# Optimization experiments

Measured on AMD Instinct MI355X. Metric: run time of the kernel, lower is better.

## Reference

```python
import jax, jax.numpy as jnp
import numpy as np

HIDDEN = 1024
HEADS = 16
HEAD_DIM = HIDDEN // HEADS


def setup_inputs() -> dict:
    key = jax.random.key(0)
    ks = jax.random.split(key, 5)
    B, T = 4, 2048
    x = jax.random.normal(ks[0], (B, T, HIDDEN), dtype=jnp.float32)
    s = 1.0 / np.sqrt(HIDDEN)
    qkv_w = jax.random.normal(ks[1], (HIDDEN, 3 * HIDDEN), dtype=jnp.float32) * s
    qkv_b = jnp.zeros((3 * HIDDEN,), dtype=jnp.float32)
    proj_w = jax.random.normal(ks[2], (HIDDEN, HIDDEN), dtype=jnp.float32) * s
    proj_b = jnp.zeros((HIDDEN,), dtype=jnp.float32)
    return {"x": x, "qkv_w": qkv_w, "qkv_b": qkv_b, "proj_w": proj_w, "proj_b": proj_b}


def reference(x, qkv_w, qkv_b, proj_w, proj_b):
    B, T, C = x.shape
    qkv = x @ qkv_w + qkv_b                       # [B,T,3C]
    qkv = qkv.reshape(B, T, 3, HEADS, HEAD_DIM)
    q, k, v = qkv[:, :, 0], qkv[:, :, 1], qkv[:, :, 2]  # [B,T,H,D]
    scale = HEAD_DIM ** -0.5
    scores = jnp.einsum('bthd,bshd->bhts', q, k) * scale  # [B,H,T,T]
    attn = jax.nn.softmax(scores, axis=-1)
    out = jnp.einsum('bhts,bshd->bthd', attn, v).reshape(B, T, C)
    return out @ proj_w + proj_b
```

## Files before the change

### kernel.cpp

```cpp
#include <hip/hip_runtime.h>
#include <hip/hip_bf16.h>

#define HID  1024
#define N3   3072
#define NH   16
#define HD   64
#define SEQ  2048
#define NB   4
#define MTOT 8192

typedef unsigned short u16x8 __attribute__((ext_vector_type(8)));
typedef unsigned short u16x4 __attribute__((ext_vector_type(4)));
typedef float f32x4 __attribute__((ext_vector_type(4)));

static __device__ __forceinline__ unsigned short f2bf(float f) {
    union { float f; unsigned u; } v; v.f = f;
    unsigned r = (v.u + 0x7fffu + ((v.u >> 16) & 1u)) >> 16;
    return (unsigned short)r;
}

static __device__ __forceinline__ float fexp2(float x) {
    float r; asm("v_exp_f32 %0, %1" : "=v"(r) : "v"(x)); return r;
}

typedef __attribute__((address_space(3))) void* lds_vp;
typedef const __attribute__((address_space(1))) void* gbl_vp;

static __device__ __forceinline__ void gload16(const void* g, void* l) {
    __builtin_amdgcn_global_load_lds((gbl_vp)g, (lds_vp)l, 16, 0, 0);
}

#define CQ 0.18033688011112042f

__global__ void k_cvt(const float* __restrict__ in, unsigned short* __restrict__ out, int n) {
    int i = (blockIdx.x * 256 + threadIdx.x) * 8;
    if (i >= n) return;
    float4 a = *(const float4*)(in + i);
    float4 b = *(const float4*)(in + i + 4);
    u16x8 p;
    p[0]=f2bf(a.x); p[1]=f2bf(a.y); p[2]=f2bf(a.z); p[3]=f2bf(a.w);
    p[4]=f2bf(b.x); p[5]=f2bf(b.y); p[6]=f2bf(b.z); p[7]=f2bf(b.w);
    *(u16x8*)(out + i) = p;
}

__global__ void k_tcvt(const float* __restrict__ W, unsigned short* __restrict__ WT, int R, int C) {
    int tiles_c = C >> 6;
    int k0 = (blockIdx.x / tiles_c) << 6;
    int n0 = (blockIdx.x % tiles_c) << 6;
    __shared__ unsigned short tile[64 * 64];
    int tid = threadIdx.x;
    #pragma unroll
    for (int it = 0; it < 2; ++it) {
        int task = it * 256 + tid;
        int t = task >> 3, dc = task & 7;
        const float* src = W + (size_t)(k0 + t) * C + n0 + dc * 8;
        float4 a = *(const float4*)src;
        float4 b = *(const float4*)(src + 4);
        u16x8 p;
        p[0]=f2bf(a.x); p[1]=f2bf(a.y); p[2]=f2bf(a.z); p[3]=f2bf(a.w);
        p[4]=f2bf(b.x); p[5]=f2bf(b.y); p[6]=f2bf(b.z); p[7]=f2bf(b.w);
        *(u16x8*)&tile[t * 64 + ((dc ^ (t & 7)) << 3)] = p;
    }
    __syncthreads();
    #pragma unroll
    for (int it = 0; it < 2; ++it) {
        int task = it * 256 + tid;
        int d = task >> 3, tc = task & 7;
        u16x8 p;
        #pragma unroll
        for (int i = 0; i < 8; ++i) {
            int ii = (i + tc) & 7;
            int t = tc * 8 + ii;
            p[ii] = tile[t * 64 + ((((d >> 3) ^ (t & 7)) << 3)) + (d & 7)];
        }
        *(u16x8*)(WT + (size_t)(n0 + d) * R + k0 + tc * 8) = p;
    }
}

template<int MODE>
__global__ __launch_bounds__(256) void k_gemm(const unsigned short* __restrict__ A,
                                              const unsigned short* __restrict__ BT,
                                              const float* __restrict__ bias,
                                              void* __restrict__ C1, void* __restrict__ C2,
                                              int M, int N, int K) {
    int tiles_n = N >> 7;
    int bid = (blockIdx.x & 7) * (gridDim.x >> 3) + (blockIdx.x >> 3);
    int bm = bid / tiles_n, bn = bid % tiles_n;
    int tid = threadIdx.x, wid = tid >> 6, lane = tid & 63;
    int wr = wid >> 1, wc = wid & 1;
    int fr = lane & 15, fg = lane >> 4;

    __shared__ unsigned short lA[128 * 64];
    __shared__ unsigned short lB[128 * 64];

    f32x4 acc[4][4];
    #pragma unroll
    for (int m = 0; m < 4; ++m)
        #pragma unroll
        for (int n = 0; n < 4; ++n)
            acc[m][n] = (f32x4){0.f, 0.f, 0.f, 0.f};

    int srow = lane >> 3;
    int sch  = (lane & 7) ^ srow;
    const unsigned short* aSrc[4]; const unsigned short* bSrc[4];
    unsigned short* aDst[4]; unsigned short* bDst[4];
    #pragma unroll
    for (int i = 0; i < 4; ++i) {
        int rbase = i * 32 + wid * 8;
        aSrc[i] = A  + (size_t)(bm * 128 + rbase + srow) * K + sch * 8;
        bSrc[i] = BT + (size_t)(bn * 128 + rbase + srow) * K + sch * 8;
        aDst[i] = lA + rbase * 64;
        bDst[i] = lB + rbase * 64;
    }

    for (int k0 = 0; k0 < K; k0 += 64) {
        __syncthreads();
        #pragma unroll
        for (int i = 0; i < 4; ++i) {
            gload16(aSrc[i] + k0, aDst[i]);
            gload16(bSrc[i] + k0, bDst[i]);
        }
        asm volatile("s_waitcnt vmcnt(0)" ::: "memory");
        __syncthreads();
        #pragma unroll
        for (int kk = 0; kk < 2; ++kk) {
            u16x8 af[4], bf[4];
            #pragma unroll
            for (int m = 0; m < 4; ++m) {
                int row = wr * 64 + m * 16 + fr;
                int ch = ((kk << 2) + fg) ^ (fr & 7);
                af[m] = *(const u16x8*)&lA[row * 64 + ch * 8];
            }
            #pragma unroll
            for (int n = 0; n < 4; ++n) {
                int row = wc * 64 + n * 16 + fr;
                int ch = ((kk << 2) + fg) ^ (fr & 7);
                bf[n] = *(const u16x8*)&lB[row * 64 + ch * 8];
            }
            #pragma unroll
            for (int m = 0; m < 4; ++m)
                #pragma unroll
                for (int n = 0; n < 4; ++n)
                    acc[m][n] = __builtin_amdgcn_mfma_f32_16x16x32_bf16(af[m], bf[n], acc[m][n], 0, 0, 0);
        }
    }

    if (MODE == 0) {
        float* C = (float*)C1;
        #pragma unroll
        for (int n = 0; n < 4; ++n) {
            int col = bn * 128 + wc * 64 + n * 16 + fr;
            float bv = bias[col];
            #pragma unroll
            for (int m = 0; m < 4; ++m) {
                int row0 = bm * 128 + wr * 64 + m * 16 + fg * 4;
                #pragma unroll
                for (int r = 0; r < 4; ++r)
                    C[(size_t)(row0 + r) * N + col] = acc[m][n][r] + bv;
            }
        }
    } else {
        if (bn < 16) {
            unsigned short* qkb = (unsigned short*)C1;
            #pragma unroll
            for (int n = 0; n < 4; ++n) {
                int col = bn * 128 + wc * 64 + n * 16 + fr;
                float bv = bias[col];
                float cs = (col < 1024) ? CQ : 1.0f;
                #pragma unroll
                for (int m = 0; m < 4; ++m) {
                    int row0 = bm * 128 + wr * 64 + m * 16 + fg * 4;
                    #pragma unroll
                    for (int r = 0; r < 4; ++r)
                        qkb[(size_t)(row0 + r) * 2048 + col] = f2bf((acc[m][n][r] + bv) * cs);
                }
            }
        } else {
            unsigned short* vT = (unsigned short*)C2;
            #pragma unroll
            for (int n = 0; n < 4; ++n) {
                int col = bn * 128 + wc * 64 + n * 16 + fr;
                float bv = bias[col];
                int cv = col - 2048;
                int hh = cv >> 6, d = cv & 63;
                #pragma unroll
                for (int m = 0; m < 4; ++m) {
                    int row0 = bm * 128 + wr * 64 + m * 16 + fg * 4;
                    int bb = row0 >> 11, t0 = row0 & 2047;
                    u16x4 st;
                    #pragma unroll
                    for (int r = 0; r < 4; ++r) st[r] = f2bf(acc[m][n][r] + bv);
                    *(u16x4*)&vT[((size_t)((bb * 16 + hh) * 64 + d)) * 2048 + t0] = st;
                }
            }
        }
    }
}

__global__ __launch_bounds__(256) void k_attn(const unsigned short* __restrict__ qkb,
                                              const unsigned short* __restrict__ vT,
                                              unsigned short* __restrict__ out) {
    int bid = (blockIdx.x & 7) * 128 + (blockIdx.x >> 3);
    int bh = bid >> 4;
    int q0 = (bid & 15) << 7;
    int b = bh >> 4, h = bh & 15;
    int tid = threadIdx.x, wid = tid >> 6, lane = tid & 63;
    int fr = lane & 15, fg = lane >> 4;

    __shared__ unsigned short lK[2][8192];
    __shared__ unsigned short lV[2][8192];
    const char* lKb = (const char*)lK;
    const char* lVb = (const char*)lV;

    int srow = lane >> 3;
    int sch  = (lane & 7) ^ srow;
    int woff = wid * 512;

    u16x8 ones;
    #pragma unroll
    for (int i = 0; i < 8; ++i) ones[i] = 0x3F80;

    int kfb[2], vbb[4];
    #pragma unroll
    for (int kk = 0; kk < 2; ++kk) kfb[kk] = fr * 128 + (((((kk << 2) + fg) ^ (fr & 7))) << 4);
    #pragma unroll
    for (int kk = 0; kk < 4; ++kk) vbb[kk] = fr * 256 + (((((kk << 2) + fg) ^ (fr & 7))) << 4);

    const unsigned short* qbase = qkb + (size_t)(b * SEQ) * 2048 + h * 64;
    #pragma unroll
    for (int i = 0; i < 4; ++i) {
        int rbase = i * 32 + wid * 8;
        gload16(qbase + (size_t)(q0 + rbase + srow) * 2048 + sch * 8, (unsigned short*)lK + rbase * 64);
    }
    asm volatile("s_waitcnt vmcnt(0)" ::: "memory");
    __syncthreads();
    u16x8 qf[2][2];
    #pragma unroll
    for (int j = 0; j < 2; ++j)
        #pragma unroll
        for (int kk = 0; kk < 2; ++kk)
            qf[j][kk] = *(const u16x8*)(lKb + kfb[kk] + (wid * 32 + j * 16) * 128);
    __syncthreads();

    f32x4 o[2][4];
    #pragma unroll
    for (int j = 0; j < 2; ++j)
        #pragma unroll
        for (int i = 0; i < 4; ++i)
            o[j][i] = (f32x4){0.f, 0.f, 0.f, 0.f};
    f32x4 o_sum[2];
    o_sum[0] = (f32x4){0.f, 0.f, 0.f, 0.f};
    o_sum[1] = (f32x4){0.f, 0.f, 0.f, 0.f};

    const unsigned short* kp[4]; const unsigned short* vp[4];
    {
        const unsigned short* kbase = qkb + (size_t)(b * SEQ) * 2048 + 1024 + h * 64;
        const unsigned short* vbase = vT + (size_t)(bh * 64) * SEQ;
        #pragma unroll
        for (int i = 0; i < 4; ++i) {
            kp[i] = kbase + (size_t)(i * 32 + wid * 8 + srow) * 2048 + sch * 8;
            int vrow = i * 16 + wid * 4 + (lane >> 4);
            int vch = (lane & 15) ^ (vrow & 7);
            vp[i] = vbase + (size_t)vrow * SEQ + vch * 8;
        }
    }

#define STAGE(bufi) do {                                                   \
        unsigned short* kd = (unsigned short*)lK + (bufi) * 8192 + woff;   \
        unsigned short* vd = (unsigned short*)lV + (bufi) * 8192 + woff;   \
        _Pragma("unroll")                                                  \
        for (int i = 0; i < 4; ++i) {                                      \
            gload16(kp[i], kd + i * 2048);  kp[i] += 128 * 2048;           \
            gload16(vp[i], vd + i * 2048);  vp[i] += 128;                  \
        }                                                                  \
    } while (0)

    STAGE(0);

    for (int t = 0; t < 16; ++t) {
        int cur = t & 1;
        int cb = cur * 16384;
        if (t < 15) {
            STAGE(cur ^ 1);
            asm volatile("s_waitcnt vmcnt(8)" ::: "memory");
        } else {
            asm volatile("s_waitcnt vmcnt(0)" ::: "memory");
        }
        __builtin_amdgcn_s_barrier();
        __builtin_amdgcn_sched_barrier(0);

        u16x8 pb[2][4];
        #pragma unroll
        for (int ih = 0; ih < 2; ++ih) {
            f32x4 sa[2][4];
            #pragma unroll
            for (int j = 0; j < 2; ++j)
                #pragma unroll
                for (int il = 0; il < 4; ++il)
                    sa[j][il] = (f32x4){0.f, 0.f, 0.f, 0.f};
            #pragma unroll
            for (int kk = 0; kk < 2; ++kk) {
                u16x8 kf[4];
                #pragma unroll
                for (int il = 0; il < 4; ++il)
                    kf[il] = *(const u16x8*)(lKb + cb + kfb[kk] + (ih * 4 + il) * 2048);
                #pragma unroll
                for (int j = 0; j < 2; ++j)
                    #pragma unroll
                    for (int il = 0; il < 4; ++il)
                        sa[j][il] = __builtin_amdgcn_mfma_f32_16x16x32_bf16(kf[il], qf[j][kk], sa[j][il], 0, 0, 0);
            }

            #pragma unroll
            for (int j = 0; j < 2; ++j) {
                unsigned pk[2][2][2];
                #pragma unroll
                for (int il = 0; il < 4; ++il) {
                    #pragma unroll
                    for (int p = 0; p < 2; ++p) {
                        float ea = fexp2(sa[j][il][2 * p]);
                        float eb = fexp2(sa[j][il][2 * p + 1]);
                        unsigned rr;
                        asm("v_cvt_pk_bf16_f32 %0, %1, %2" : "=v"(rr) : "v"(ea), "v"(eb));
                        pk[il >> 1][il & 1][p] = rr;
                    }
                }
                #pragma unroll
                for (int t2 = 0; t2 < 2; ++t2) {
                    #pragma unroll
                    for (int p = 0; p < 2; ++p) {
                        asm("v_permlane32_swap_b32 %0, %1" : "+v"(pk[t2][0][p]), "+v"(pk[t2][1][p]));
                        asm("v_permlane16_swap_b32 %0, %1" : "+v"(pk[t2][0][p]), "+v"(pk[t2][1][p]));
                    }
                    union { unsigned u[4]; u16x8 v; } w;
                    w.u[0] = pk[t2][0][0]; w.u[1] = pk[t2][0][1];
                    w.u[2] = pk[t2][1][0]; w.u[3] = pk[t2][1][1];
                    pb[j][ih * 2 + t2] = w.v;
                    o_sum[j] = __builtin_amdgcn_mfma_f32_16x16x32_bf16(ones, pb[j][ih * 2 + t2], o_sum[j], 0, 0, 0);
                }
            }
        }

        #pragma unroll
        for (int kk = 0; kk < 4; ++kk) {
            u16x8 vb[4];
            #pragma unroll
            for (int i = 0; i < 4; ++i)
                vb[i] = *(const u16x8*)(lVb + cb + vbb[kk] + i * 4096);
            #pragma unroll
            for (int j = 0; j < 2; ++j)
                #pragma unroll
                for (int i = 0; i < 4; ++i)
                    o[j][i] = __builtin_amdgcn_mfma_f32_16x16x32_bf16(vb[i], pb[j][kk], o[j][i], 0, 0, 0);
        }

        __syncthreads();
    }
#undef STAGE

    #pragma unroll
    for (int j = 0; j < 2; ++j) {
        float inv = 1.f / o_sum[j][0];
        size_t t = q0 + wid * 32 + j * 16 + fr;
        #pragma unroll
        for (int i = 0; i < 4; ++i) {
            u16x4 st;
            st[0] = f2bf(o[j][i][0] * inv);
            st[1] = f2bf(o[j][i][1] * inv);
            st[2] = f2bf(o[j][i][2] * inv);
            st[3] = f2bf(o[j][i][3] * inv);
            *(u16x4*)&out[(size_t)(b * SEQ + t) * HID + h * 64 + i * 16 + fg * 4] = st;
        }
    }
}

extern "C" void kernel_launch(void* const* d_in, const int* in_sizes, int n_in,
                              void* d_out, int out_size, void* d_ws, size_t ws_size,
                              hipStream_t stream) {
    const float* x      = (const float*)d_in[0];
    const float* qkv_w  = (const float*)d_in[1];
    const float* qkv_b  = (const float*)d_in[2];
    const float* proj_w = (const float*)d_in[3];
    const float* proj_b = (const float*)d_in[4];
    float* out = (float*)d_out;

    char* ws = (char*)d_ws;
    unsigned short* xb     = (unsigned short*)ws;
    unsigned short* wqkvT  = (unsigned short*)(ws + 16777216);
    unsigned short* wprojT = (unsigned short*)(ws + 23068672);
    unsigned short* qkb    = (unsigned short*)(ws + 25165824);
    unsigned short* vTb    = (unsigned short*)(ws + 58720256);
    unsigned short* aob    = (unsigned short*)(ws + 75497472);

    k_cvt<<<4096, 256, 0, stream>>>(x, xb, MTOT * HID);
    k_tcvt<<<768, 256, 0, stream>>>(qkv_w, wqkvT, HID, N3);
    k_tcvt<<<256, 256, 0, stream>>>(proj_w, wprojT, HID, HID);
    k_gemm<1><<<1536, 256, 0, stream>>>(xb, wqkvT, qkv_b, (void*)qkb, (void*)vTb, MTOT, N3, HID);
    k_attn<<<1024, 256, 0, stream>>>(qkb, vTb, aob);
    k_gemm<0><<<512, 256, 0, stream>>>(aob, wprojT, proj_b, (void*)out, nullptr, MTOT, HID, HID);
}
```

Measured before the change: 201.9 us.

## Double attention query tile per block to 256 rows and restructure inner loop

```diff
diff --git a/kernel.cpp b/kernel.cpp
--- a/kernel.cpp
+++ b/kernel.cpp
@@ -200,9 +200,9 @@
 __global__ __launch_bounds__(256) void k_attn(const unsigned short* __restrict__ qkb,
                                               const unsigned short* __restrict__ vT,
                                               unsigned short* __restrict__ out) {
-    int bid = (blockIdx.x & 7) * 128 + (blockIdx.x >> 3);
-    int bh = bid >> 4;
-    int q0 = (bid & 15) << 7;
+    int bid = (blockIdx.x & 7) * 64 + (blockIdx.x >> 3);
+    int bh = bid >> 3;
+    int q0 = (bid & 7) << 8;
     int b = bh >> 4, h = bh & 15;
     int tid = threadIdx.x, wid = tid >> 6, lane = tid & 63;
     int fr = lane & 15, fg = lane >> 4;
@@ -228,29 +228,29 @@
 
     const unsigned short* qbase = qkb + (size_t)(b * SEQ) * 2048 + h * 64;
     #pragma unroll
-    for (int i = 0; i < 4; ++i) {
+    for (int i = 0; i < 8; ++i) {
         int rbase = i * 32 + wid * 8;
         gload16(qbase + (size_t)(q0 + rbase + srow) * 2048 + sch * 8, (unsigned short*)lK + rbase * 64);
     }
     asm volatile("s_waitcnt vmcnt(0)" ::: "memory");
     __syncthreads();
-    u16x8 qf[2][2];
-    #pragma unroll
-    for (int j = 0; j < 2; ++j)
+    u16x8 qf[4][2];
+    #pragma unroll
+    for (int j = 0; j < 4; ++j)
         #pragma unroll
         for (int kk = 0; kk < 2; ++kk)
-            qf[j][kk] = *(const u16x8*)(lKb + kfb[kk] + (wid * 32 + j * 16) * 128);
+            qf[j][kk] = *(const u16x8*)(lKb + kfb[kk] + (wid * 64 + j * 16) * 128);
     __syncthreads();
 
-    f32x4 o[2][4];
-    #pragma unroll
-    for (int j = 0; j < 2; ++j)
+    f32x4 o[4][4];
+    #pragma unroll
+    for (int j = 0; j < 4; ++j)
         #pragma unroll
         for (int i = 0; i < 4; ++i)
             o[j][i] = (f32x4){0.f, 0.f, 0.f, 0.f};
-    f32x4 o_sum[2];
-    o_sum[0] = (f32x4){0.f, 0.f, 0.f, 0.f};
-    o_sum[1] = (f32x4){0.f, 0.f, 0.f, 0.f};
+    f32x4 o_sum[4];
+    #pragma unroll
+    for (int j = 0; j < 4; ++j) o_sum[j] = (f32x4){0.f, 0.f, 0.f, 0.f};
 
     const unsigned short* kp[4]; const unsigned short* vp[4];
     {
@@ -289,40 +289,38 @@
         __builtin_amdgcn_s_barrier();
         __builtin_amdgcn_sched_barrier(0);
 
-        u16x8 pb[2][4];
-        #pragma unroll
-        for (int ih = 0; ih < 2; ++ih) {
-            f32x4 sa[2][4];
-            #pragma unroll
-            for (int j = 0; j < 2; ++j)
-                #pragma unroll
-                for (int il = 0; il < 4; ++il)
-                    sa[j][il] = (f32x4){0.f, 0.f, 0.f, 0.f};
+        #pragma unroll
+        for (int j = 0; j < 4; ++j) {
+            f32x4 sa[8];
+            #pragma unroll
+            for (int il = 0; il < 8; ++il) sa[il] = (f32x4){0.f, 0.f, 0.f, 0.f};
             #pragma unroll
             for (int kk = 0; kk < 2; ++kk) {
-                u16x8 kf[4];
-                #pragma unroll
-                for (int il = 0; il < 4; ++il)
-                    kf[il] = *(const u16x8*)(lKb + cb + kfb[kk] + (ih * 4 + il) * 2048);
-                #pragma unroll
-                for (int j = 0; j < 2; ++j)
-                    #pragma unroll
-                    for (int il = 0; il < 4; ++il)
-                        sa[j][il] = __builtin_amdgcn_mfma_f32_16x16x32_bf16(kf[il], qf[j][kk], sa[j][il], 0, 0, 0);
-            }
-
-            #pragma unroll
-            for (int j = 0; j < 2; ++j) {
+                u16x8 kf[8];
+                #pragma unroll
+                for (int il = 0; il < 8; ++il)
+                    kf[il] = *(const u16x8*)(lKb + cb + kfb[kk] + il * 2048);
+                __builtin_amdgcn_s_setprio(1);
+                #pragma unroll
+                for (int il = 0; il < 8; ++il)
+                    sa[il] = __builtin_amdgcn_mfma_f32_16x16x32_bf16(kf[il], qf[j][kk], sa[il], 0, 0, 0);
+                __builtin_amdgcn_s_setprio(0);
+            }
+
+            u16x8 pb[4];
+            #pragma unroll
+            for (int ih = 0; ih < 2; ++ih) {
                 unsigned pk[2][2][2];
                 #pragma unroll
-                for (int il = 0; il < 4; ++il) {
+                for (int i4 = 0; i4 < 4; ++i4) {
+                    int il = ih * 4 + i4;
                     #pragma unroll
                     for (int p = 0; p < 2; ++p) {
-                        float ea = fexp2(sa[j][il][2 * p]);
-                        float eb = fexp2(sa[j][il][2 * p + 1]);
+                        float ea = fexp2(sa[il][2 * p]);
+                        float eb = fexp2(sa[il][2 * p + 1]);
                         unsigned rr;
                         asm("v_cvt_pk_bf16_f32 %0, %1, %2" : "=v"(rr) : "v"(ea), "v"(eb));
-                        pk[il >> 1][il & 1][p] = rr;
+                        pk[i4 >> 1][i4 & 1][p] = rr;
                     }
                 }
                 #pragma unroll
@@ -335,23 +333,23 @@
                     union { unsigned u[4]; u16x8 v; } w;
                     w.u[0] = pk[t2][0][0]; w.u[1] = pk[t2][0][1];
                     w.u[2] = pk[t2][1][0]; w.u[3] = pk[t2][1][1];
-                    pb[j][ih * 2 + t2] = w.v;
-                    o_sum[j] = __builtin_amdgcn_mfma_f32_16x16x32_bf16(ones, pb[j][ih * 2 + t2], o_sum[j], 0, 0, 0);
+                    pb[ih * 2 + t2] = w.v;
                 }
             }
-        }
-
-        #pragma unroll
-        for (int kk = 0; kk < 4; ++kk) {
-            u16x8 vb[4];
-            #pragma unroll
-            for (int i = 0; i < 4; ++i)
-                vb[i] = *(const u16x8*)(lVb + cb + vbb[kk] + i * 4096);
-            #pragma unroll
-            for (int j = 0; j < 2; ++j)
+
+            #pragma unroll
+            for (int kk = 0; kk < 4; ++kk) {
+                u16x8 vb[4];
                 #pragma unroll
                 for (int i = 0; i < 4; ++i)
-                    o[j][i] = __builtin_amdgcn_mfma_f32_16x16x32_bf16(vb[i], pb[j][kk], o[j][i], 0, 0, 0);
+                    vb[i] = *(const u16x8*)(lVb + cb + vbb[kk] + i * 4096);
+                __builtin_amdgcn_s_setprio(1);
+                o_sum[j] = __builtin_amdgcn_mfma_f32_16x16x32_bf16(ones, pb[kk], o_sum[j], 0, 0, 0);
+                #pragma unroll
+                for (int i = 0; i < 4; ++i)
+                    o[j][i] = __builtin_amdgcn_mfma_f32_16x16x32_bf16(vb[i], pb[kk], o[j][i], 0, 0, 0);
+                __builtin_amdgcn_s_setprio(0);
+            }
         }
 
         __syncthreads();
@@ -359,9 +357,9 @@
 #undef STAGE
 
     #pragma unroll
-    for (int j = 0; j < 2; ++j) {
+    for (int j = 0; j < 4; ++j) {
         float inv = 1.f / o_sum[j][0];
-        size_t t = q0 + wid * 32 + j * 16 + fr;
+        size_t t = q0 + wid * 64 + j * 16 + fr;
         #pragma unroll
         for (int i = 0; i < 4; ++i) {
             u16x4 st;
@@ -396,6 +394,6 @@
     k_tcvt<<<768, 256, 0, stream>>>(qkv_w, wqkvT, HID, N3);
     k_tcvt<<<256, 256, 0, stream>>>(proj_w, wprojT, HID, HID);
     k_gemm<1><<<1536, 256, 0, stream>>>(xb, wqkvT, qkv_b, (void*)qkb, (void*)vTb, MTOT, N3, HID);
-    k_attn<<<1024, 256, 0, stream>>>(qkb, vTb, aob);
+    k_attn<<<512, 256, 0, stream>>>(qkb, vTb, aob);
     k_gemm<0><<<512, 256, 0, stream>>>(aob, wprojT, proj_b, (void*)out, nullptr, MTOT, HID, HID);
 }
```

Result: no change. 202.8 us (+0.4%).
